# Kernel optimization log

Measured on AMD Instinct MI355X. Metric: run time of the kernel, lower is better.

Reference implementation:

```python
import jax, jax.numpy as jnp
import numpy as np

N_NODES = 100000
HIDDEN = 64
N_EDGES = 1600000


def _sage_conv(x, edge_index, Wl, Wr, b):
    # PyG SAGEConv (mean aggr): out_i = W_l @ mean_{j->i} x_j + W_r @ x_i + b
    src, dst = edge_index[0], edge_index[1]
    msg = x[src]                                      # [E, H] gather
    agg = jax.ops.segment_sum(msg, dst, num_segments=N_NODES)  # [N, H]
    deg = jax.ops.segment_sum(jnp.ones((msg.shape[0],), x.dtype), dst,
                              num_segments=N_NODES)
    agg = agg / jnp.maximum(deg, 1.0)[:, None]
    return agg @ Wl.T + x @ Wr.T + b


def setup_inputs() -> dict:
    key = jax.random.key(0)
    ks = jax.random.split(key, 8)
    s = 1.0 / np.sqrt(HIDDEN)
    return {
        "emb": jax.random.normal(ks[0], (N_NODES, HIDDEN), jnp.float32),
        "Wl1": jax.random.normal(ks[1], (HIDDEN, HIDDEN), jnp.float32) * s,
        "Wr1": jax.random.normal(ks[2], (HIDDEN, HIDDEN), jnp.float32) * s,
        "b1": jnp.zeros((HIDDEN,), jnp.float32),
        "Wl2": jax.random.normal(ks[3], (HIDDEN, HIDDEN), jnp.float32) * s,
        "Wr2": jax.random.normal(ks[4], (HIDDEN, HIDDEN), jnp.float32) * s,
        "b2": jnp.zeros((HIDDEN,), jnp.float32),
        "node_id": jnp.arange(N_NODES, dtype=jnp.int64 if jax.config.jax_enable_x64 else jnp.int32),
        "edge_index": jax.random.randint(ks[5], (2, N_EDGES), 0, N_NODES),
    }


def reference(emb, Wl1, Wr1, b1, Wl2, Wr2, b2, node_id, edge_index):
    # Embedding lookup
    x = emb[node_id]                                   # [N, H]
    # GNN: relu(conv1) -> conv2
    x = jax.nn.relu(_sage_conv(x, edge_index, Wl1, Wr1, b1))
    x = _sage_conv(x, edge_index, Wl2, Wr2, b2)
    # Classifier: per-edge dot product of endpoint features
    ef1 = x[edge_index[0]]                             # [E, H]
    ef2 = x[edge_index[1]]                             # [E, H]
    return (ef1 * ef2).sum(axis=-1)                    # [E]
```

## Files before the change

### kernel.cpp

```cpp
#include <hip/hip_runtime.h>

#define N_NODES 100000
#define HID 64
#define N_EDGES 1600000
#define NB 391
#define NBP 392
#define NHB 250
#define C_EPB 6400
#define GATHER_BLOCKS 6250

typedef __attribute__((ext_vector_type(8))) short bf16x8;
typedef __attribute__((ext_vector_type(4))) float f32x4;

__device__ __forceinline__ unsigned short f2bf(float f) {
    unsigned u = __float_as_uint(f);
    u = (u + 0x7FFFu + ((u >> 16) & 1u)) >> 16;
    return (unsigned short)u;
}
__device__ __forceinline__ float bflo(unsigned w) { return __uint_as_float(w << 16); }
__device__ __forceinline__ float bfhi(unsigned w) { return __uint_as_float(w & 0xFFFF0000u); }

__global__ void gather_hist_kernel(const float* __restrict__ emb,
                                   const int* __restrict__ nid,
                                   unsigned short* __restrict__ xh,
                                   const int* __restrict__ dst,
                                   int* __restrict__ bhist_part) {
    if (blockIdx.x < GATHER_BLOCKS) {
        int i = blockIdx.x * blockDim.x + threadIdx.x;
        const int total = N_NODES * (HID / 4);
        if (i >= total) return;
        int row = i >> 4;
        int c   = i & 15;
        int s   = nid[row];
        float4 v = reinterpret_cast<const float4*>(emb)[(size_t)s * 16 + c];
        uint2 p;
        p.x = (unsigned)f2bf(v.x) | ((unsigned)f2bf(v.y) << 16);
        p.y = (unsigned)f2bf(v.z) | ((unsigned)f2bf(v.w) << 16);
        reinterpret_cast<uint2*>(xh)[(size_t)row * 16 + c] = p;
        return;
    }
    __shared__ int h[NB];
    for (int i = threadIdx.x; i < NB; i += blockDim.x) h[i] = 0;
    __syncthreads();
    int hb = blockIdx.x - GATHER_BLOCKS;
    const int4* d4 = (const int4*)dst;
    int q0 = hb * (C_EPB / 4);
    int q1 = q0 + (C_EPB / 4);
    for (int q = q0 + threadIdx.x; q < q1; q += blockDim.x) {
        int4 v = d4[q];
        atomicAdd(&h[v.x >> 8], 1);
        atomicAdd(&h[v.y >> 8], 1);
        atomicAdd(&h[v.z >> 8], 1);
        atomicAdd(&h[v.w >> 8], 1);
    }
    __syncthreads();
    for (int i = threadIdx.x; i < NB; i += blockDim.x)
        bhist_part[hb * NBP + i] = h[i];
}

__global__ void bucket_scan(const int* __restrict__ bhist_part,
                            int* __restrict__ boff,
                            int* __restrict__ bcursor) {
    __shared__ int s[512];
    int v = 0;
    if (threadIdx.x < NB) {
        #pragma unroll 8
        for (int p = 0; p < NHB; ++p) v += bhist_part[p * NBP + threadIdx.x];
    }
    s[threadIdx.x] = v;
    __syncthreads();
    for (int off = 1; off < 512; off <<= 1) {
        int t = (threadIdx.x >= off) ? s[threadIdx.x - off] : 0;
        __syncthreads();
        s[threadIdx.x] += t;
        __syncthreads();
    }
    if (threadIdx.x < NB) {
        int ex = s[threadIdx.x] - v;
        boff[threadIdx.x] = ex;
        bcursor[threadIdx.x] = ex;
    }
}

__global__ void bucket_scatter(const int* __restrict__ src,
                               const int* __restrict__ dst,
                               const int* __restrict__ bhist_part,
                               int* __restrict__ bcursor,
                               int* __restrict__ pairs) {
    __shared__ int h[NB];
    __shared__ int base[NB];
    int blk = blockIdx.x;
    for (int i = threadIdx.x; i < NB; i += blockDim.x) {
        int c = bhist_part[blk * NBP + i];
        base[i] = c ? atomicAdd(&bcursor[i], c) : 0;
        h[i] = 0;
    }
    __syncthreads();
    int e0 = blk * C_EPB;
    int e1 = e0 + C_EPB;
    for (int e = e0 + threadIdx.x; e < e1; e += blockDim.x) {
        int d = dst[e];
        int b = d >> 8;
        int slot = base[b] + atomicAdd(&h[b], 1);
        pairs[slot] = (src[e] << 8) | (d & 255);
    }
}

__global__ void bucket_csr(const int* __restrict__ pairs,
                           const int* __restrict__ boff,
                           const int* __restrict__ bcursor,
                           int* __restrict__ row_start,
                           int* __restrict__ adj) {
    __shared__ int cnt[256];
    __shared__ int sc[256];
    int b = blockIdx.x;
    int node0 = b << 8;
    int p0 = boff[b];
    int p1 = bcursor[b];
    int t = threadIdx.x;
    if (t < 256) cnt[t] = 0;
    __syncthreads();
    for (int p = p0 + t; p < p1; p += 1024)
        atomicAdd(&cnt[pairs[p] & 255], 1);
    __syncthreads();
    int v = (t < 256) ? cnt[t] : 0;
    if (t < 256) sc[t] = v;
    __syncthreads();
    for (int off = 1; off < 256; off <<= 1) {
        int u = (t >= off && t < 256) ? sc[t - off] : 0;
        __syncthreads();
        if (t < 256) sc[t] += u;
        __syncthreads();
    }
    if (t < 256) {
        sc[t] = p0 + sc[t] - v;
        int node = node0 + t;
        if (node <= N_NODES) row_start[node] = sc[t];
    }
    __syncthreads();
    for (int p = p0 + t; p < p1; p += 1024) {
        int pr = pairs[p];
        int slot = atomicAdd(&sc[pr & 255], 1);
        adj[slot] = (int)(((unsigned)pr) >> 8);
    }
}

__global__ void agg_kernel(const int* __restrict__ row_start,
                           const int* __restrict__ adj,
                           const unsigned short* __restrict__ xh,
                           unsigned short* __restrict__ M) {
    int lane = threadIdx.x & 63;
    int g = lane >> 3;
    int c = lane & 7;
    int wpb = blockDim.x >> 6;
    int wid = blockIdx.x * wpb + (threadIdx.x >> 6);
    int stride = gridDim.x * wpb;
    const uint4* xw = (const uint4*)xh;
    uint4* Mw = (uint4*)M;
    const int NQ = N_NODES / 8;
    for (int q = wid; q < NQ; q += stride) {
        int row = q * 8 + g;
        int beg = row_start[row], end = row_start[row + 1];
        float a0 = 0.f, a1 = 0.f, a2 = 0.f, a3 = 0.f;
        float a4 = 0.f, a5 = 0.f, a6 = 0.f, a7 = 0.f;
        int j = beg;
        for (; j + 7 < end; j += 8) {
            int s0 = adj[j],     s1 = adj[j + 1], s2 = adj[j + 2], s3 = adj[j + 3];
            int s4 = adj[j + 4], s5 = adj[j + 5], s6 = adj[j + 6], s7 = adj[j + 7];
            uint4 v0 = xw[(size_t)s0 * 8 + c];
            uint4 v1 = xw[(size_t)s1 * 8 + c];
            uint4 v2 = xw[(size_t)s2 * 8 + c];
            uint4 v3 = xw[(size_t)s3 * 8 + c];
            uint4 v4 = xw[(size_t)s4 * 8 + c];
            uint4 v5 = xw[(size_t)s5 * 8 + c];
            uint4 v6 = xw[(size_t)s6 * 8 + c];
            uint4 v7 = xw[(size_t)s7 * 8 + c];
            a0 += bflo(v0.x) + bflo(v1.x) + bflo(v2.x) + bflo(v3.x)
                + bflo(v4.x) + bflo(v5.x) + bflo(v6.x) + bflo(v7.x);
            a1 += bfhi(v0.x) + bfhi(v1.x) + bfhi(v2.x) + bfhi(v3.x)
                + bfhi(v4.x) + bfhi(v5.x) + bfhi(v6.x) + bfhi(v7.x);
            a2 += bflo(v0.y) + bflo(v1.y) + bflo(v2.y) + bflo(v3.y)
                + bflo(v4.y) + bflo(v5.y) + bflo(v6.y) + bflo(v7.y);
            a3 += bfhi(v0.y) + bfhi(v1.y) + bfhi(v2.y) + bfhi(v3.y)
                + bfhi(v4.y) + bfhi(v5.y) + bfhi(v6.y) + bfhi(v7.y);
            a4 += bflo(v0.z) + bflo(v1.z) + bflo(v2.z) + bflo(v3.z)
                + bflo(v4.z) + bflo(v5.z) + bflo(v6.z) + bflo(v7.z);
            a5 += bfhi(v0.z) + bfhi(v1.z) + bfhi(v2.z) + bfhi(v3.z)
                + bfhi(v4.z) + bfhi(v5.z) + bfhi(v6.z) + bfhi(v7.z);
            a6 += bflo(v0.w) + bflo(v1.w) + bflo(v2.w) + bflo(v3.w)
                + bflo(v4.w) + bflo(v5.w) + bflo(v6.w) + bflo(v7.w);
            a7 += bfhi(v0.w) + bfhi(v1.w) + bfhi(v2.w) + bfhi(v3.w)
                + bfhi(v4.w) + bfhi(v5.w) + bfhi(v6.w) + bfhi(v7.w);
        }
        if (j + 3 < end) {
            int s0 = adj[j], s1 = adj[j + 1], s2 = adj[j + 2], s3 = adj[j + 3];
            uint4 v0 = xw[(size_t)s0 * 8 + c];
            uint4 v1 = xw[(size_t)s1 * 8 + c];
            uint4 v2 = xw[(size_t)s2 * 8 + c];
            uint4 v3 = xw[(size_t)s3 * 8 + c];
            a0 += bflo(v0.x) + bflo(v1.x) + bflo(v2.x) + bflo(v3.x);
            a1 += bfhi(v0.x) + bfhi(v1.x) + bfhi(v2.x) + bfhi(v3.x);
            a2 += bflo(v0.y) + bflo(v1.y) + bflo(v2.y) + bflo(v3.y);
            a3 += bfhi(v0.y) + bfhi(v1.y) + bfhi(v2.y) + bfhi(v3.y);
            a4 += bflo(v0.z) + bflo(v1.z) + bflo(v2.z) + bflo(v3.z);
            a5 += bfhi(v0.z) + bfhi(v1.z) + bfhi(v2.z) + bfhi(v3.z);
            a6 += bflo(v0.w) + bflo(v1.w) + bflo(v2.w) + bflo(v3.w);
            a7 += bfhi(v0.w) + bfhi(v1.w) + bfhi(v2.w) + bfhi(v3.w);
            j += 4;
        }
        for (; j < end; ++j) {
            uint4 v = xw[(size_t)adj[j] * 8 + c];
            a0 += bflo(v.x); a1 += bfhi(v.x);
            a2 += bflo(v.y); a3 += bfhi(v.y);
            a4 += bflo(v.z); a5 += bfhi(v.z);
            a6 += bflo(v.w); a7 += bfhi(v.w);
        }
        float inv = 1.0f / fmaxf((float)(end - beg), 1.0f);
        uint4 p;
        p.x = (unsigned)f2bf(a0 * inv) | ((unsigned)f2bf(a1 * inv) << 16);
        p.y = (unsigned)f2bf(a2 * inv) | ((unsigned)f2bf(a3 * inv) << 16);
        p.z = (unsigned)f2bf(a4 * inv) | ((unsigned)f2bf(a5 * inv) << 16);
        p.w = (unsigned)f2bf(a6 * inv) | ((unsigned)f2bf(a7 * inv) << 16);
        Mw[(size_t)row * 8 + c] = p;
    }
}

__global__ void gemm_kernel(const unsigned short* __restrict__ Am,
                            const unsigned short* __restrict__ As,
                            const float* __restrict__ Wl,
                            const float* __restrict__ Wr,
                            const float* __restrict__ bias,
                            unsigned short* __restrict__ H,
                            int relu) {
    int lane = threadIdx.x & 63;
    int m = lane & 15, quad = lane >> 4;

    bf16x8 wf[2][2][4];
    for (int mat = 0; mat < 2; ++mat) {
        const float* W = mat ? Wr : Wl;
        for (int ks = 0; ks < 2; ++ks)
            for (int ct = 0; ct < 4; ++ct) {
                const float* p = W + (ct * 16 + m) * HID + ks * 32 + quad * 8;
                bf16x8 f;
                #pragma unroll
                for (int j = 0; j < 8; ++j) f[j] = (short)f2bf(p[j]);
                wf[mat][ks][ct] = f;
            }
    }
    float bv[4];
    #pragma unroll
    for (int ct = 0; ct < 4; ++ct) bv[ct] = bias[ct * 16 + m];

    int wpb = blockDim.x >> 6;
    int wid = blockIdx.x * wpb + (threadIdx.x >> 6);
    int stride = gridDim.x * wpb;
    const int NT = N_NODES / 16;
    for (int t = wid; t < NT; t += stride) {
        f32x4 acc[4] = {{0,0,0,0},{0,0,0,0},{0,0,0,0},{0,0,0,0}};
        size_t rowbase = ((size_t)t * 16 + m) * HID;
        #pragma unroll
        for (int ks = 0; ks < 2; ++ks) {
            bf16x8 a0 = *(const bf16x8*)(Am + rowbase + ks * 32 + quad * 8);
            bf16x8 a1 = *(const bf16x8*)(As + rowbase + ks * 32 + quad * 8);
            #pragma unroll
            for (int ct = 0; ct < 4; ++ct) {
                acc[ct] = __builtin_amdgcn_mfma_f32_16x16x32_bf16(a0, wf[0][ks][ct], acc[ct], 0, 0, 0);
                acc[ct] = __builtin_amdgcn_mfma_f32_16x16x32_bf16(a1, wf[1][ks][ct], acc[ct], 0, 0, 0);
            }
        }
        #pragma unroll
        for (int ct = 0; ct < 4; ++ct) {
            #pragma unroll
            for (int r = 0; r < 4; ++r) {
                float v = acc[ct][r] + bv[ct];
                if (relu) v = fmaxf(v, 0.f);
                H[((size_t)t * 16 + quad * 4 + r) * HID + ct * 16 + m] = f2bf(v);
            }
        }
    }
}

__global__ void edge_dot_kernel(const int* __restrict__ src,
                                const int* __restrict__ dst,
                                const unsigned short* __restrict__ h,
                                float* __restrict__ out) {
    int t = blockIdx.x * blockDim.x + threadIdx.x;
    int g = t >> 3;
    int c = t & 7;
    int e0 = g * 2;
    if (e0 >= N_EDGES) return;
    int a0 = src[e0],     b0 = dst[e0];
    int a1 = src[e0 + 1], b1 = dst[e0 + 1];
    const uint4* h4 = reinterpret_cast<const uint4*>(h);
    uint4 va0 = h4[(size_t)a0 * 8 + c];
    uint4 vb0 = h4[(size_t)b0 * 8 + c];
    uint4 va1 = h4[(size_t)a1 * 8 + c];
    uint4 vb1 = h4[(size_t)b1 * 8 + c];
    float p0 = bflo(va0.x) * bflo(vb0.x) + bfhi(va0.x) * bfhi(vb0.x)
             + bflo(va0.y) * bflo(vb0.y) + bfhi(va0.y) * bfhi(vb0.y)
             + bflo(va0.z) * bflo(vb0.z) + bfhi(va0.z) * bfhi(vb0.z)
             + bflo(va0.w) * bflo(vb0.w) + bfhi(va0.w) * bfhi(vb0.w);
    float p1 = bflo(va1.x) * bflo(vb1.x) + bfhi(va1.x) * bfhi(vb1.x)
             + bflo(va1.y) * bflo(vb1.y) + bfhi(va1.y) * bfhi(vb1.y)
             + bflo(va1.z) * bflo(vb1.z) + bfhi(va1.z) * bfhi(vb1.z)
             + bflo(va1.w) * bflo(vb1.w) + bfhi(va1.w) * bfhi(vb1.w);
    p0 += __shfl_xor(p0, 1); p0 += __shfl_xor(p0, 2); p0 += __shfl_xor(p0, 4);
    p1 += __shfl_xor(p1, 1); p1 += __shfl_xor(p1, 2); p1 += __shfl_xor(p1, 4);
    if (c == 0) reinterpret_cast<float2*>(out)[g] = make_float2(p0, p1);
}

extern "C" void kernel_launch(void* const* d_in, const int* in_sizes, int n_in,
                              void* d_out, int out_size, void* d_ws, size_t ws_size,
                              hipStream_t stream) {
    const float* emb = (const float*)d_in[0];
    const float* Wl1 = (const float*)d_in[1];
    const float* Wr1 = (const float*)d_in[2];
    const float* b1  = (const float*)d_in[3];
    const float* Wl2 = (const float*)d_in[4];
    const float* Wr2 = (const float*)d_in[5];
    const float* b2  = (const float*)d_in[6];
    const int*   nid = (const int*)d_in[7];
    const int*   ei  = (const int*)d_in[8];
    const int* esrc = ei;
    const int* edst = ei + N_EDGES;
    float* out = (float*)d_out;

    const size_t NH = (size_t)N_NODES * HID;
    unsigned short* xh  = (unsigned short*)d_ws;
    unsigned short* h1h = xh + NH;
    unsigned short* h2h = h1h + NH;
    unsigned short* M   = h2h + NH;
    int* ib        = (int*)(M + NH);
    int* row_start = ib;
    int* adj       = ib + N_NODES + 64;
    int* pairs     = adj + N_EDGES + 64;
    int* bhist_part = pairs + N_EDGES;
    int* boff      = bhist_part + NHB * NBP;
    int* bcursor   = boff + NB + 1;

    gather_hist_kernel<<<GATHER_BLOCKS + NHB, 256, 0, stream>>>(emb, nid, xh, edst, bhist_part);

    bucket_scan<<<1, 512, 0, stream>>>(bhist_part, boff, bcursor);
    bucket_scatter<<<NHB, 1024, 0, stream>>>(esrc, edst, bhist_part, bcursor, pairs);
    bucket_csr<<<NB, 1024, 0, stream>>>(pairs, boff, bcursor, row_start, adj);

    agg_kernel<<<2048, 256, 0, stream>>>(row_start, adj, xh, M);
    gemm_kernel<<<512, 256, 0, stream>>>(M, xh, Wl1, Wr1, b1, h1h, 1);

    agg_kernel<<<2048, 256, 0, stream>>>(row_start, adj, h1h, M);
    gemm_kernel<<<512, 256, 0, stream>>>(M, h1h, Wl2, Wr2, b2, h2h, 0);

    edge_dot_kernel<<<((size_t)(N_EDGES / 2) * 8 + 255) / 256, 256, 0, stream>>>(esrc, edst, h2h, out);
}
```

Measured before the change: 269.9 us.

## Fuse neighbor aggregation with MFMA projection and prepack bf16 weights in prep kernel

```diff
diff --git a/kernel.cpp b/kernel.cpp
--- a/kernel.cpp
+++ b/kernel.cpp
@@ -20,11 +20,16 @@
 __device__ __forceinline__ float bflo(unsigned w) { return __uint_as_float(w << 16); }
 __device__ __forceinline__ float bfhi(unsigned w) { return __uint_as_float(w & 0xFFFF0000u); }
 
-__global__ void gather_hist_kernel(const float* __restrict__ emb,
-                                   const int* __restrict__ nid,
-                                   unsigned short* __restrict__ xh,
-                                   const int* __restrict__ dst,
-                                   int* __restrict__ bhist_part) {
+__global__ void prep_kernel(const float* __restrict__ emb,
+                            const int* __restrict__ nid,
+                            unsigned short* __restrict__ xh,
+                            const int* __restrict__ dst,
+                            int* __restrict__ bhist_part,
+                            const float* __restrict__ Wl1,
+                            const float* __restrict__ Wr1,
+                            const float* __restrict__ Wl2,
+                            const float* __restrict__ Wr2,
+                            unsigned short* __restrict__ wpack) {
     if (blockIdx.x < GATHER_BLOCKS) {
         int i = blockIdx.x * blockDim.x + threadIdx.x;
         const int total = N_NODES * (HID / 4);
@@ -39,23 +44,41 @@
         reinterpret_cast<uint2*>(xh)[(size_t)row * 16 + c] = p;
         return;
     }
-    __shared__ int h[NB];
-    for (int i = threadIdx.x; i < NB; i += blockDim.x) h[i] = 0;
-    __syncthreads();
-    int hb = blockIdx.x - GATHER_BLOCKS;
-    const int4* d4 = (const int4*)dst;
-    int q0 = hb * (C_EPB / 4);
-    int q1 = q0 + (C_EPB / 4);
-    for (int q = q0 + threadIdx.x; q < q1; q += blockDim.x) {
-        int4 v = d4[q];
-        atomicAdd(&h[v.x >> 8], 1);
-        atomicAdd(&h[v.y >> 8], 1);
-        atomicAdd(&h[v.z >> 8], 1);
-        atomicAdd(&h[v.w >> 8], 1);
-    }
-    __syncthreads();
-    for (int i = threadIdx.x; i < NB; i += blockDim.x)
-        bhist_part[hb * NBP + i] = h[i];
+    if (blockIdx.x < GATHER_BLOCKS + NHB) {
+        __shared__ int h[NB];
+        for (int i = threadIdx.x; i < NB; i += blockDim.x) h[i] = 0;
+        __syncthreads();
+        int hb = blockIdx.x - GATHER_BLOCKS;
+        const int4* d4 = (const int4*)dst;
+        int q0 = hb * (C_EPB / 4);
+        int q1 = q0 + (C_EPB / 4);
+        for (int q = q0 + threadIdx.x; q < q1; q += blockDim.x) {
+            int4 v = d4[q];
+            atomicAdd(&h[v.x >> 8], 1);
+            atomicAdd(&h[v.y >> 8], 1);
+            atomicAdd(&h[v.z >> 8], 1);
+            atomicAdd(&h[v.w >> 8], 1);
+        }
+        __syncthreads();
+        for (int i = threadIdx.x; i < NB; i += blockDim.x)
+            bhist_part[hb * NBP + i] = h[i];
+        return;
+    }
+    int L = blockIdx.x - GATHER_BLOCKS - NHB;
+    const float* WL = L ? Wl2 : Wl1;
+    const float* WR = L ? Wr2 : Wr1;
+    for (int idx = threadIdx.x; idx < 1024; idx += 256) {
+        int lane = idx & 63;
+        int ct   = (idx >> 6) & 3;
+        int ks   = (idx >> 8) & 1;
+        int mat  = idx >> 9;
+        const float* W = mat ? WR : WL;
+        int m = lane & 15, quad = lane >> 4;
+        const float* p = W + (ct * 16 + m) * HID + ks * 32 + quad * 8;
+        unsigned short* q = wpack + ((size_t)L * 1024 + idx) * 8;
+        #pragma unroll
+        for (int j = 0; j < 8; ++j) q[j] = f2bf(p[j]);
+    }
 }
 
 __global__ void bucket_scan(const int* __restrict__ bhist_part,
@@ -145,127 +168,114 @@
     }
 }
 
-__global__ void agg_kernel(const int* __restrict__ row_start,
-                           const int* __restrict__ adj,
-                           const unsigned short* __restrict__ xh,
-                           unsigned short* __restrict__ M) {
+__global__ void sage_fused_kernel(const int* __restrict__ row_start,
+                                  const int* __restrict__ adj,
+                                  const unsigned short* __restrict__ X,
+                                  const unsigned short* __restrict__ wpack,
+                                  const float* __restrict__ bias,
+                                  unsigned short* __restrict__ H,
+                                  int relu) {
+    __shared__ uint4 lds4[4 * 16 * 8];
     int lane = threadIdx.x & 63;
+    int w    = threadIdx.x >> 6;
     int g = lane >> 3;
     int c = lane & 7;
+    int m    = lane & 15;
+    int quad = lane >> 4;
     int wpb = blockDim.x >> 6;
-    int wid = blockIdx.x * wpb + (threadIdx.x >> 6);
+    int wid = blockIdx.x * wpb + w;
     int stride = gridDim.x * wpb;
-    const uint4* xw = (const uint4*)xh;
-    uint4* Mw = (uint4*)M;
-    const int NQ = N_NODES / 8;
-    for (int q = wid; q < NQ; q += stride) {
-        int row = q * 8 + g;
-        int beg = row_start[row], end = row_start[row + 1];
-        float a0 = 0.f, a1 = 0.f, a2 = 0.f, a3 = 0.f;
-        float a4 = 0.f, a5 = 0.f, a6 = 0.f, a7 = 0.f;
-        int j = beg;
-        for (; j + 7 < end; j += 8) {
-            int s0 = adj[j],     s1 = adj[j + 1], s2 = adj[j + 2], s3 = adj[j + 3];
-            int s4 = adj[j + 4], s5 = adj[j + 5], s6 = adj[j + 6], s7 = adj[j + 7];
-            uint4 v0 = xw[(size_t)s0 * 8 + c];
-            uint4 v1 = xw[(size_t)s1 * 8 + c];
-            uint4 v2 = xw[(size_t)s2 * 8 + c];
-            uint4 v3 = xw[(size_t)s3 * 8 + c];
-            uint4 v4 = xw[(size_t)s4 * 8 + c];
-            uint4 v5 = xw[(size_t)s5 * 8 + c];
-            uint4 v6 = xw[(size_t)s6 * 8 + c];
-            uint4 v7 = xw[(size_t)s7 * 8 + c];
-            a0 += bflo(v0.x) + bflo(v1.x) + bflo(v2.x) + bflo(v3.x)
-                + bflo(v4.x) + bflo(v5.x) + bflo(v6.x) + bflo(v7.x);
-            a1 += bfhi(v0.x) + bfhi(v1.x) + bfhi(v2.x) + bfhi(v3.x)
-                + bfhi(v4.x) + bfhi(v5.x) + bfhi(v6.x) + bfhi(v7.x);
-            a2 += bflo(v0.y) + bflo(v1.y) + bflo(v2.y) + bflo(v3.y)
-                + bflo(v4.y) + bflo(v5.y) + bflo(v6.y) + bflo(v7.y);
-            a3 += bfhi(v0.y) + bfhi(v1.y) + bfhi(v2.y) + bfhi(v3.y)
-                + bfhi(v4.y) + bfhi(v5.y) + bfhi(v6.y) + bfhi(v7.y);
-            a4 += bflo(v0.z) + bflo(v1.z) + bflo(v2.z) + bflo(v3.z)
-                + bflo(v4.z) + bflo(v5.z) + bflo(v6.z) + bflo(v7.z);
-            a5 += bfhi(v0.z) + bfhi(v1.z) + bfhi(v2.z) + bfhi(v3.z)
-                + bfhi(v4.z) + bfhi(v5.z) + bfhi(v6.z) + bfhi(v7.z);
-            a6 += bflo(v0.w) + bflo(v1.w) + bflo(v2.w) + bflo(v3.w)
-                + bflo(v4.w) + bflo(v5.w) + bflo(v6.w) + bflo(v7.w);
-            a7 += bfhi(v0.w) + bfhi(v1.w) + bfhi(v2.w) + bfhi(v3.w)
-                + bfhi(v4.w) + bfhi(v5.w) + bfhi(v6.w) + bfhi(v7.w);
-        }
-        if (j + 3 < end) {
-            int s0 = adj[j], s1 = adj[j + 1], s2 = adj[j + 2], s3 = adj[j + 3];
-            uint4 v0 = xw[(size_t)s0 * 8 + c];
-            uint4 v1 = xw[(size_t)s1 * 8 + c];
-            uint4 v2 = xw[(size_t)s2 * 8 + c];
-            uint4 v3 = xw[(size_t)s3 * 8 + c];
-            a0 += bflo(v0.x) + bflo(v1.x) + bflo(v2.x) + bflo(v3.x);
-            a1 += bfhi(v0.x) + bfhi(v1.x) + bfhi(v2.x) + bfhi(v3.x);
-            a2 += bflo(v0.y) + bflo(v1.y) + bflo(v2.y) + bflo(v3.y);
-            a3 += bfhi(v0.y) + bfhi(v1.y) + bfhi(v2.y) + bfhi(v3.y);
-            a4 += bflo(v0.z) + bflo(v1.z) + bflo(v2.z) + bflo(v3.z);
-            a5 += bfhi(v0.z) + bfhi(v1.z) + bfhi(v2.z) + bfhi(v3.z);
-            a6 += bflo(v0.w) + bflo(v1.w) + bflo(v2.w) + bflo(v3.w);
-            a7 += bfhi(v0.w) + bfhi(v1.w) + bfhi(v2.w) + bfhi(v3.w);
-            j += 4;
-        }
-        for (; j < end; ++j) {
-            uint4 v = xw[(size_t)adj[j] * 8 + c];
-            a0 += bflo(v.x); a1 += bfhi(v.x);
-            a2 += bflo(v.y); a3 += bfhi(v.y);
-            a4 += bflo(v.z); a5 += bfhi(v.z);
-            a6 += bflo(v.w); a7 += bfhi(v.w);
-        }
-        float inv = 1.0f / fmaxf((float)(end - beg), 1.0f);
-        uint4 p;
-        p.x = (unsigned)f2bf(a0 * inv) | ((unsigned)f2bf(a1 * inv) << 16);
-        p.y = (unsigned)f2bf(a2 * inv) | ((unsigned)f2bf(a3 * inv) << 16);
-        p.z = (unsigned)f2bf(a4 * inv) | ((unsigned)f2bf(a5 * inv) << 16);
-        p.w = (unsigned)f2bf(a6 * inv) | ((unsigned)f2bf(a7 * inv) << 16);
-        Mw[(size_t)row * 8 + c] = p;
-    }
-}
-
-__global__ void gemm_kernel(const unsigned short* __restrict__ Am,
-                            const unsigned short* __restrict__ As,
-                            const float* __restrict__ Wl,
-                            const float* __restrict__ Wr,
-                            const float* __restrict__ bias,
-                            unsigned short* __restrict__ H,
-                            int relu) {
-    int lane = threadIdx.x & 63;
-    int m = lane & 15, quad = lane >> 4;
-
-    bf16x8 wf[2][2][4];
-    for (int mat = 0; mat < 2; ++mat) {
-        const float* W = mat ? Wr : Wl;
-        for (int ks = 0; ks < 2; ++ks)
-            for (int ct = 0; ct < 4; ++ct) {
-                const float* p = W + (ct * 16 + m) * HID + ks * 32 + quad * 8;
-                bf16x8 f;
-                #pragma unroll
-                for (int j = 0; j < 8; ++j) f[j] = (short)f2bf(p[j]);
-                wf[mat][ks][ct] = f;
-            }
-    }
+    const int NT = N_NODES / 16;
+    const uint4* xw = (const uint4*)X;
+    const bf16x8* wp = (const bf16x8*)wpack;
+    uint4* myl = lds4 + w * 128;
     float bv[4];
     #pragma unroll
     for (int ct = 0; ct < 4; ++ct) bv[ct] = bias[ct * 16 + m];
 
-    int wpb = blockDim.x >> 6;
-    int wid = blockIdx.x * wpb + (threadIdx.x >> 6);
-    int stride = gridDim.x * wpb;
-    const int NT = N_NODES / 16;
     for (int t = wid; t < NT; t += stride) {
+        #pragma unroll
+        for (int half = 0; half < 2; ++half) {
+            int row = t * 16 + half * 8 + g;
+            int beg = row_start[row], end = row_start[row + 1];
+            float a0 = 0.f, a1 = 0.f, a2 = 0.f, a3 = 0.f;
+            float a4 = 0.f, a5 = 0.f, a6 = 0.f, a7 = 0.f;
+            int j = beg;
+            for (; j + 7 < end; j += 8) {
+                int s0 = adj[j],     s1 = adj[j + 1], s2 = adj[j + 2], s3 = adj[j + 3];
+                int s4 = adj[j + 4], s5 = adj[j + 5], s6 = adj[j + 6], s7 = adj[j + 7];
+                uint4 v0 = xw[(size_t)s0 * 8 + c];
+                uint4 v1 = xw[(size_t)s1 * 8 + c];
+                uint4 v2 = xw[(size_t)s2 * 8 + c];
+                uint4 v3 = xw[(size_t)s3 * 8 + c];
+                uint4 v4 = xw[(size_t)s4 * 8 + c];
+                uint4 v5 = xw[(size_t)s5 * 8 + c];
+                uint4 v6 = xw[(size_t)s6 * 8 + c];
+                uint4 v7 = xw[(size_t)s7 * 8 + c];
+                a0 += bflo(v0.x) + bflo(v1.x) + bflo(v2.x) + bflo(v3.x)
+                    + bflo(v4.x) + bflo(v5.x) + bflo(v6.x) + bflo(v7.x);
+                a1 += bfhi(v0.x) + bfhi(v1.x) + bfhi(v2.x) + bfhi(v3.x)
+                    + bfhi(v4.x) + bfhi(v5.x) + bfhi(v6.x) + bfhi(v7.x);
+                a2 += bflo(v0.y) + bflo(v1.y) + bflo(v2.y) + bflo(v3.y)
+                    + bflo(v4.y) + bflo(v5.y) + bflo(v6.y) + bflo(v7.y);
+                a3 += bfhi(v0.y) + bfhi(v1.y) + bfhi(v2.y) + bfhi(v3.y)
+                    + bfhi(v4.y) + bfhi(v5.y) + bfhi(v6.y) + bfhi(v7.y);
+                a4 += bflo(v0.z) + bflo(v1.z) + bflo(v2.z) + bflo(v3.z)
+                    + bflo(v4.z) + bflo(v5.z) + bflo(v6.z) + bflo(v7.z);
+                a5 += bfhi(v0.z) + bfhi(v1.z) + bfhi(v2.z) + bfhi(v3.z)
+                    + bfhi(v4.z) + bfhi(v5.z) + bfhi(v6.z) + bfhi(v7.z);
+                a6 += bflo(v0.w) + bflo(v1.w) + bflo(v2.w) + bflo(v3.w)
+                    + bflo(v4.w) + bflo(v5.w) + bflo(v6.w) + bflo(v7.w);
+                a7 += bfhi(v0.w) + bfhi(v1.w) + bfhi(v2.w) + bfhi(v3.w)
+                    + bfhi(v4.w) + bfhi(v5.w) + bfhi(v6.w) + bfhi(v7.w);
+            }
+            if (j + 3 < end) {
+                int s0 = adj[j], s1 = adj[j + 1], s2 = adj[j + 2], s3 = adj[j + 3];
+                uint4 v0 = xw[(size_t)s0 * 8 + c];
+                uint4 v1 = xw[(size_t)s1 * 8 + c];
+                uint4 v2 = xw[(size_t)s2 * 8 + c];
+                uint4 v3 = xw[(size_t)s3 * 8 + c];
+                a0 += bflo(v0.x) + bflo(v1.x) + bflo(v2.x) + bflo(v3.x);
+                a1 += bfhi(v0.x) + bfhi(v1.x) + bfhi(v2.x) + bfhi(v3.x);
+                a2 += bflo(v0.y) + bflo(v1.y) + bflo(v2.y) + bflo(v3.y);
+                a3 += bfhi(v0.y) + bfhi(v1.y) + bfhi(v2.y) + bfhi(v3.y);
+                a4 += bflo(v0.z) + bflo(v1.z) + bflo(v2.z) + bflo(v3.z);
+                a5 += bfhi(v0.z) + bfhi(v1.z) + bfhi(v2.z) + bfhi(v3.z);
+                a6 += bflo(v0.w) + bflo(v1.w) + bflo(v2.w) + bflo(v3.w);
+                a7 += bfhi(v0.w) + bfhi(v1.w) + bfhi(v2.w) + bfhi(v3.w);
+                j += 4;
+            }
+            for (; j < end; ++j) {
+                uint4 v = xw[(size_t)adj[j] * 8 + c];
+                a0 += bflo(v.x); a1 += bfhi(v.x);
+                a2 += bflo(v.y); a3 += bfhi(v.y);
+                a4 += bflo(v.z); a5 += bfhi(v.z);
+                a6 += bflo(v.w); a7 += bfhi(v.w);
+            }
+            float inv = 1.0f / fmaxf((float)(end - beg), 1.0f);
+            uint4 p;
+            p.x = (unsigned)f2bf(a0 * inv) | ((unsigned)f2bf(a1 * inv) << 16);
+            p.y = (unsigned)f2bf(a2 * inv) | ((unsigned)f2bf(a3 * inv) << 16);
+            p.z = (unsigned)f2bf(a4 * inv) | ((unsigned)f2bf(a5 * inv) << 16);
+            p.w = (unsigned)f2bf(a6 * inv) | ((unsigned)f2bf(a7 * inv) << 16);
+            myl[(half * 8 + g) * 8 + c] = p;
+        }
+        bf16x8 am0 = *reinterpret_cast<const bf16x8*>(&myl[m * 8 + quad]);
+        bf16x8 am1 = *reinterpret_cast<const bf16x8*>(&myl[m * 8 + 4 + quad]);
+        int row = t * 16 + m;
+        bf16x8 as0 = *(const bf16x8*)(X + (size_t)row * HID + quad * 8);
+        bf16x8 as1 = *(const bf16x8*)(X + (size_t)row * HID + 32 + quad * 8);
         f32x4 acc[4] = {{0,0,0,0},{0,0,0,0},{0,0,0,0},{0,0,0,0}};
-        size_t rowbase = ((size_t)t * 16 + m) * HID;
         #pragma unroll
         for (int ks = 0; ks < 2; ++ks) {
-            bf16x8 a0 = *(const bf16x8*)(Am + rowbase + ks * 32 + quad * 8);
-            bf16x8 a1 = *(const bf16x8*)(As + rowbase + ks * 32 + quad * 8);
+            bf16x8 amean = ks ? am1 : am0;
+            bf16x8 aself = ks ? as1 : as0;
             #pragma unroll
             for (int ct = 0; ct < 4; ++ct) {
-                acc[ct] = __builtin_amdgcn_mfma_f32_16x16x32_bf16(a0, wf[0][ks][ct], acc[ct], 0, 0, 0);
-                acc[ct] = __builtin_amdgcn_mfma_f32_16x16x32_bf16(a1, wf[1][ks][ct], acc[ct], 0, 0, 0);
+                acc[ct] = __builtin_amdgcn_mfma_f32_16x16x32_bf16(
+                    amean, wp[(size_t)ks * 256 + ct * 64 + lane], acc[ct], 0, 0, 0);
+                acc[ct] = __builtin_amdgcn_mfma_f32_16x16x32_bf16(
+                    aself, wp[(size_t)512 + ks * 256 + ct * 64 + lane], acc[ct], 0, 0, 0);
             }
         }
         #pragma unroll
@@ -329,26 +339,26 @@
     unsigned short* xh  = (unsigned short*)d_ws;
     unsigned short* h1h = xh + NH;
     unsigned short* h2h = h1h + NH;
-    unsigned short* M   = h2h + NH;
-    int* ib        = (int*)(M + NH);
+    int* ib        = (int*)(h2h + NH);
     int* row_start = ib;
     int* adj       = ib + N_NODES + 64;
     int* pairs     = adj + N_EDGES + 64;
     int* bhist_part = pairs + N_EDGES;
     int* boff      = bhist_part + NHB * NBP;
     int* bcursor   = boff + NB + 1;
-
-    gather_hist_kernel<<<GATHER_BLOCKS + NHB, 256, 0, stream>>>(emb, nid, xh, edst, bhist_part);
+    unsigned short* wpack = (unsigned short*)(bcursor + NB + 1);
+
+    prep_kernel<<<GATHER_BLOCKS + NHB + 2, 256, 0, stream>>>(
+        emb, nid, xh, edst, bhist_part, Wl1, Wr1, Wl2, Wr2, wpack);
 
     bucket_scan<<<1, 512, 0, stream>>>(bhist_part, boff, bcursor);
     bucket_scatter<<<NHB, 1024, 0, stream>>>(esrc, edst, bhist_part, bcursor, pairs);
     bucket_csr<<<NB, 1024, 0, stream>>>(pairs, boff, bcursor, row_start, adj);
 
-    agg_kernel<<<2048, 256, 0, stream>>>(row_start, adj, xh, M);
-    gemm_kernel<<<512, 256, 0, stream>>>(M, xh, Wl1, Wr1, b1, h1h, 1);
-
-    agg_kernel<<<2048, 256, 0, stream>>>(row_start, adj, h1h, M);
-    gemm_kernel<<<512, 256, 0, stream>>>(M, h1h, Wl2, Wr2, b2, h2h, 0);
+    sage_fused_kernel<<<2048, 256, 0, stream>>>(row_start, adj, xh,
+                                                wpack, b1, h1h, 1);
+    sage_fused_kernel<<<2048, 256, 0, stream>>>(row_start, adj, h1h,
+                                                wpack + 1024 * 8, b2, h2h, 0);
 
     edge_dot_kernel<<<((size_t)(N_EDGES / 2) * 8 + 255) / 256, 256, 0, stream>>>(esrc, edst, h2h, out);
 }
```

Measured after the change: 272.3 us. About the same (+0.9%).
